# Kernel optimization log

Measured on AMD Instinct MI355X. Metric: run time of the kernel, lower is better.

Reference implementation:

```python
import jax, jax.numpy as jnp
import numpy as np

C = 64  # channels fixed by module

def conv1x1(x, W, b):
    # x: [B,C,H,W], W: [C_out,C_in], b: [C_out]
    return jnp.einsum('bchw,oc->bohw', x, W) + b[None, :, None, None]

def setup_inputs() -> dict:
    key = jax.random.key(0)
    ks = jax.random.split(key, 16)
    B, H, W = 4, 64, 64
    inp = {
        'x_latter': jax.random.normal(ks[0], (B, C, H, W), jnp.float32),
        'x': jax.random.normal(ks[1], (B, C, H, W), jnp.float32),
    }
    scale = 1.0 / np.sqrt(C)
    names = ['high', 'low', 'value', 'e_conv', 'mid', 'latter']
    for i, n in enumerate(names):
        inp[f'W_{n}'] = jax.random.normal(ks[2 + 2 * i], (C, C), jnp.float32) * scale
        inp[f'b_{n}'] = jax.random.normal(ks[3 + 2 * i], (C,), jnp.float32) * 0.01
    return inp

def reference(x_latter, x, W_high, b_high, W_low, b_low, W_value, b_value,
              W_e_conv, b_e_conv, W_mid, b_mid, W_latter, b_latter):
    b, c, h, w = x_latter.shape
    hw = h * w
    # stage 1: channel-normalized spatial attention
    xl_hi = conv1x1(x_latter, W_high, b_high).reshape(b, c, hw)          # [b,c,hw]
    x_low = conv1x1(x, W_low, b_low).reshape(b, c, hw).transpose(0, 2, 1)  # [b,hw,c]
    p = jnp.einsum('bnc,bcm->bnm', x_low, xl_hi)                          # [b,hw,hw]
    p = jax.nn.softmax(p, axis=1)  # torch Softmax(dim=1) over first hw axis
    v = conv1x1(x, W_value, b_value).reshape(b, c, hw).transpose(0, 2, 1)  # [b,hw,c]
    e = jnp.einsum('bnm,bmc->bnc', p, v) + x_low                          # [b,hw,c]
    e = e.transpose(0, 2, 1).reshape(b, c, h, w)                          # [b,c,h,w]
    e = conv1x1(e, W_e_conv, b_e_conv).reshape(b, c, hw)                  # [b,c,hw]
    # stage 2: channel-channel attention
    xl2 = conv1x1(x_latter, W_latter, b_latter).reshape(b, c, hw).transpose(0, 2, 1)  # [b,hw,c]
    t = jnp.einsum('bcn,bnd->bcd', e, xl2)                                # [b,c,c]
    t = jax.nn.softmax(t, axis=1)
    x_mid = conv1x1(x, W_mid, b_mid).reshape(b, c, hw).transpose(0, 2, 1)  # [b,hw,c]
    out = jnp.einsum('bnc,bcd->bnd', x_mid, t)                            # [b,hw,c]
    return out.transpose(0, 2, 1).reshape(b, c, h, w)
```

## Files before the change

### kernel.cpp

```cpp
#include <hip/hip_runtime.h>
#include <math.h>

#define BATCH 4
#define CH 64
#define HW 4096

typedef __attribute__((ext_vector_type(8))) short short8;
typedef __attribute__((ext_vector_type(4))) float f32x4;
typedef __attribute__((ext_vector_type(4))) float float4v;

#define MFMA(a, b, c) __builtin_amdgcn_mfma_f32_16x16x32_bf16(a, b, c, 0, 0, 0)

__device__ __forceinline__ short f2bf(float f) {
    unsigned u = __builtin_bit_cast(unsigned, f);
    u += 0x7fffu + ((u >> 16) & 1u);
    return (short)(u >> 16);
}
__device__ __forceinline__ float bf2f(short s) {
    unsigned u = ((unsigned)(unsigned short)s) << 16;
    return __builtin_bit_cast(float, u);
}
__device__ __forceinline__ void gld16(const short* g, short* l) {
    __builtin_amdgcn_global_load_lds(
        (const __attribute__((address_space(1))) unsigned int*)g,
        (__attribute__((address_space(3))) unsigned int*)l, 16, 0, 0);
}

__global__ __launch_bounds__(256) void splitX(
    const float* __restrict__ x, const float* __restrict__ xl,
    short* __restrict__ XFh, short* __restrict__ XFl)
{
    int src = blockIdx.z, b = blockIdx.y, bx = blockIdx.x;
    const float* X = src ? xl : x;
    int t = threadIdx.x, wv = t >> 6, ln = t & 63;
    int nt = bx * 4 + wv;
    int n = (nt << 4) + (ln & 15);
    int g = ln >> 4;
    size_t sb = ((size_t)(src * BATCH + b) * 256 + nt) * 2;
    #pragma unroll
    for (int kt = 0; kt < 2; kt++) {
        short8 h, l;
        #pragma unroll
        for (int j = 0; j < 8; j++) {
            float v = X[(size_t)(b * 64 + kt * 32 + g * 8 + j) * HW + n];
            short hh = f2bf(v);
            h[j] = hh;
            l[j] = f2bf(v - bf2f(hh));
        }
        *(short8*)(XFh + (sb + kt) * 512 + (size_t)ln * 8) = h;
        *(short8*)(XFl + (sb + kt) * 512 + (size_t)ln * 8) = l;
    }
}

__global__ __launch_bounds__(256) void convm(
    const short* __restrict__ XFh, const short* __restrict__ XFl,
    const float* __restrict__ Wlow, const float* __restrict__ blow,
    const float* __restrict__ Wval, const float* __restrict__ bval,
    const float* __restrict__ Wmid, const float* __restrict__ bmid,
    const float* __restrict__ Wlat, const float* __restrict__ blat,
    const float* __restrict__ Whigh, const float* __restrict__ bhigh,
    float* __restrict__ XLOW, float* __restrict__ XMID, float* __restrict__ XL2,
    short* __restrict__ PAh, short* __restrict__ PAl,
    short* __restrict__ PBh, short* __restrict__ PBl,
    short* __restrict__ PVh, short* __restrict__ PVl)
{
    int mode = blockIdx.z, b = blockIdx.y, bx = blockIdx.x;
    const float* W; const float* bias; int src;
    switch (mode) {
        case 0:  W = Wlow;  bias = blow;  src = 0; break;
        case 1:  W = Wval;  bias = bval;  src = 0; break;
        case 2:  W = Wmid;  bias = bmid;  src = 0; break;
        case 3:  W = Wlat;  bias = blat;  src = 1; break;
        default: W = Whigh; bias = bhigh; src = 1; break;
    }
    int t = threadIdx.x, wv = t >> 6, ln = t & 63;
    int row = ln & 15, g = ln >> 4;

    short8 Wh[4][2], Wlo[4][2];
    #pragma unroll
    for (int ot = 0; ot < 4; ot++)
        #pragma unroll
        for (int kt = 0; kt < 2; kt++) {
            const float* wp = W + (ot * 16 + row) * 64 + kt * 32 + g * 8;
            short8 h, l;
            #pragma unroll
            for (int j = 0; j < 8; j++) {
                float v = wp[j];
                short hh = f2bf(v);
                h[j] = hh;
                l[j] = f2bf(v - bf2f(hh));
            }
            Wh[ot][kt] = h; Wlo[ot][kt] = l;
        }

    int nt = bx * 4 + wv;
    size_t xb = ((size_t)(src * BATCH + b) * 256 + nt) * 2;
    short8 Bh[2], Bl[2];
    #pragma unroll
    for (int kt = 0; kt < 2; kt++) {
        Bh[kt] = *(const short8*)(XFh + (xb + kt) * 512 + (size_t)ln * 8);
        Bl[kt] = *(const short8*)(XFl + (xb + kt) * 512 + (size_t)ln * 8);
    }

    f32x4 acc[4];
    #pragma unroll
    for (int ot = 0; ot < 4; ot++) {
        #pragma unroll
        for (int r = 0; r < 4; r++) acc[ot][r] = bias[ot * 16 + g * 4 + r];
    }
    #pragma unroll
    for (int ot = 0; ot < 4; ot++)
        #pragma unroll
        for (int kt = 0; kt < 2; kt++) {
            acc[ot] = MFMA(Wh[ot][kt], Bh[kt], acc[ot]);
            acc[ot] = MFMA(Wh[ot][kt], Bl[kt], acc[ot]);
            acc[ot] = MFMA(Wlo[ot][kt], Bh[kt], acc[ot]);
        }

    __shared__ float Ld[64][65];
    #pragma unroll
    for (int ot = 0; ot < 4; ot++)
        #pragma unroll
        for (int r = 0; r < 4; r++)
            Ld[wv * 16 + (ln & 15)][ot * 16 + g * 4 + r] = acc[ot][r];
    __syncthreads();

    int n0 = bx * 64;
    if (mode == 0 || mode == 2 || mode == 3) {
        float* outp = (mode == 0) ? XLOW : (mode == 2) ? XMID : XL2;
        int n = t >> 2, o0 = (t & 3) * 16;
        float vout[16];
        #pragma unroll
        for (int k = 0; k < 16; k++) vout[k] = Ld[n][o0 + k];
        float* gp = outp + ((size_t)b * HW + n0 + n) * 64 + o0;
        #pragma unroll
        for (int k = 0; k < 4; k++)
            *(float4v*)(gp + k * 4) = *(float4v*)(vout + k * 4);
    }
    if (mode == 0 || mode == 4) {
        short* Ph = (mode == 0) ? PAh : PBh;
        short* Pl = (mode == 0) ? PAl : PBl;
        #pragma unroll
        for (int kt = 0; kt < 2; kt++) {
            short8 h, l;
            #pragma unroll
            for (int j = 0; j < 8; j++) {
                float v = Ld[wv * 16 + (ln & 15)][kt * 32 + g * 8 + j];
                short hh = f2bf(v);
                h[j] = hh;
                l[j] = f2bf(v - bf2f(hh));
            }
            size_t blob = (((size_t)b * 256 + bx * 4 + wv) * 2 + kt) * 512 + (size_t)ln * 8;
            *(short8*)(Ph + blob) = h;
            *(short8*)(Pl + blob) = l;
        }
    }
    if (mode == 1) {
        int ktm_l = wv >> 1;
        int ct0 = (wv & 1) * 2;
        #pragma unroll
        for (int cc = 0; cc < 2; cc++) {
            int ct = ct0 + cc;
            int c = ct * 16 + (ln & 15);
            short8 h, l;
            #pragma unroll
            for (int j = 0; j < 8; j++) {
                float v = Ld[(ktm_l * 2 + (j >> 2)) * 16 + g * 4 + (j & 3)][c];
                short hh = f2bf(v);
                h[j] = hh;
                l[j] = f2bf(v - bf2f(hh));
            }
            size_t blob = (((size_t)b * 128 + bx * 2 + ktm_l) * 4 + ct) * 512 + (size_t)ln * 8;
            *(short8*)(PVh + blob) = h;
            *(short8*)(PVl + blob) = l;
        }
    }
}

__global__ __launch_bounds__(256) void zpass2(
    const short* __restrict__ PAh, const short* __restrict__ PAl,
    const short* __restrict__ PBh, const short* __restrict__ PBl,
    float* __restrict__ Zp)
{
    int bid = blockIdx.x;
    int sw = (bid & 7) * 128 + (bid >> 3);
    int mchunk = sw & 63, nc = (sw >> 6) & 3, b = sw >> 8;
    int t = threadIdx.x, wv = t >> 6, ln = t & 63;
    short8 bh[4][2], bl[4][2];
    #pragma unroll
    for (int msub = 0; msub < 4; msub++)
        #pragma unroll
        for (int kt = 0; kt < 2; kt++) {
            size_t o = ((size_t)(b * 256 + mchunk * 4 + msub) * 2 + kt) * 512 + ln * 8;
            bh[msub][kt] = *(const short8*)(PBh + o);
            bl[msub][kt] = *(const short8*)(PBl + o);
        }
    float zacc[4] = {0.f, 0.f, 0.f, 0.f};
    for (int s = 0; s < 16; s++) {
        int nt = nc * 64 + s * 4 + wv;
        size_t ab = ((size_t)(b * 256 + nt) * 2) * 512 + ln * 8;
        short8 ah0 = *(const short8*)(PAh + ab);
        short8 ah1 = *(const short8*)(PAh + ab + 512);
        short8 al0 = *(const short8*)(PAl + ab);
        short8 al1 = *(const short8*)(PAl + ab + 512);
        #pragma unroll
        for (int msub = 0; msub < 4; msub++) {
            f32x4 acc = {0.f, 0.f, 0.f, 0.f};
            acc = MFMA(ah0, bh[msub][0], acc);
            acc = MFMA(ah1, bh[msub][1], acc);
            acc = MFMA(ah0, bl[msub][0], acc);
            acc = MFMA(ah1, bl[msub][1], acc);
            acc = MFMA(al0, bh[msub][0], acc);
            acc = MFMA(al1, bh[msub][1], acc);
            zacc[msub] += __expf(acc[0]) + __expf(acc[1]) + __expf(acc[2]) + __expf(acc[3]);
        }
    }
    #pragma unroll
    for (int msub = 0; msub < 4; msub++) {
        zacc[msub] += __shfl_xor(zacc[msub], 16, 64);
        zacc[msub] += __shfl_xor(zacc[msub], 32, 64);
    }
    __shared__ float sZ[4][64];
    if (ln < 16) {
        #pragma unroll
        for (int msub = 0; msub < 4; msub++) sZ[wv][msub * 16 + ln] = zacc[msub];
    }
    __syncthreads();
    if (t < 64) {
        float z = sZ[0][t] + sZ[1][t] + sZ[2][t] + sZ[3][t];
        Zp[((size_t)(b * 4 + nc)) * 4096 + mchunk * 64 + t] = z;
    }
}

__global__ __launch_bounds__(256) void zmerge(
    const float* __restrict__ Zp, float* __restrict__ Zi)
{
    int gi = blockIdx.x * 256 + threadIdx.x;
    int b = gi >> 12, m = gi & 4095;
    float z = 0.f;
    #pragma unroll
    for (int nc2 = 0; nc2 < 4; nc2++) z += Zp[((size_t)(b * 4 + nc2)) * 4096 + m];
    Zi[gi] = 1.f / z;
}

__global__ __launch_bounds__(256) void epass5(
    const short* __restrict__ PAh, const short* __restrict__ PAl,
    const short* __restrict__ PBh, const short* __restrict__ PBl,
    const short* __restrict__ PVh, const short* __restrict__ PVl,
    const float* __restrict__ Zi, float* __restrict__ Ep)
{
    int bid = blockIdx.x;
    int sw = (bid & 7) * 64 + (bid >> 3);
    int b = sw >> 7, mseg = (sw >> 5) & 3, nb = sw & 31;
    int t = threadIdx.x, wv = t >> 6, ln = t & 63;
    int lnm = ln & 15, lnr = ln >> 4;

    __shared__ __align__(16) short sB[2][2][4096];
    __shared__ __align__(16) short sV[2][2][4096];
    __shared__ float sZi[1024];

    for (int k = t; k < 1024; k += 256) sZi[k] = Zi[b * 4096 + mseg * 1024 + k];
    __syncthreads();

    short8 Lh[2][2], Ll[2][2];
    #pragma unroll
    for (int rt = 0; rt < 2; rt++)
        #pragma unroll
        for (int kt = 0; kt < 2; kt++) {
            int nt = nb * 8 + wv * 2 + rt;
            size_t base = ((size_t)(b * 256 + nt) * 2 + kt) * 512 + ln * 8;
            Lh[rt][kt] = *(const short8*)(PAh + base);
            Ll[rt][kt] = *(const short8*)(PAl + base);
        }

    f32x4 acc_e[2][4];
    #pragma unroll
    for (int rt = 0; rt < 2; rt++)
        #pragma unroll
        for (int ct = 0; ct < 4; ct++) acc_e[rt][ct] = (f32x4){0.f, 0.f, 0.f, 0.f};

    const int mc0 = mseg * 16;
    #define STAGE(bufi, ii) { \
        size_t bb = (size_t)b * 262144 + (size_t)(mc0 + (ii)) * 4096; \
        gld16(PBh + bb + t * 8,        &sB[bufi][0][wv * 512]); \
        gld16(PBh + bb + 2048 + t * 8, &sB[bufi][0][2048 + wv * 512]); \
        gld16(PBl + bb + t * 8,        &sB[bufi][1][wv * 512]); \
        gld16(PBl + bb + 2048 + t * 8, &sB[bufi][1][2048 + wv * 512]); \
        gld16(PVh + bb + t * 8,        &sV[bufi][0][wv * 512]); \
        gld16(PVh + bb + 2048 + t * 8, &sV[bufi][0][2048 + wv * 512]); \
        gld16(PVl + bb + t * 8,        &sV[bufi][1][wv * 512]); \
        gld16(PVl + bb + 2048 + t * 8, &sV[bufi][1][2048 + wv * 512]); }

    STAGE(0, 0);
    for (int i = 0; i < 16; i++) {
        int cur = i & 1;
        __builtin_amdgcn_s_barrier();
        if (i < 15) {
            STAGE(cur ^ 1, i + 1);
            asm volatile("s_waitcnt vmcnt(8)" ::: "memory");
        } else {
            asm volatile("s_waitcnt vmcnt(0)" ::: "memory");
        }
        __builtin_amdgcn_sched_barrier(0);

        f32x4 wf[2][4];
        #pragma unroll
        for (int msub = 0; msub < 4; msub++) {
            const short8 bh0 = *(const short8*)&sB[cur][0][(msub * 2 + 0) * 512 + ln * 8];
            const short8 bh1 = *(const short8*)&sB[cur][0][(msub * 2 + 1) * 512 + ln * 8];
            const short8 bl0 = *(const short8*)&sB[cur][1][(msub * 2 + 0) * 512 + ln * 8];
            const short8 bl1 = *(const short8*)&sB[cur][1][(msub * 2 + 1) * 512 + ln * 8];
            const f32x4 vz = *(const f32x4*)&sZi[i * 64 + msub * 16 + lnr * 4];
            #pragma unroll
            for (int rt = 0; rt < 2; rt++) {
                f32x4 acc = {0.f, 0.f, 0.f, 0.f};
                acc = MFMA(bh0, Lh[rt][0], acc);
                acc = MFMA(bh1, Lh[rt][1], acc);
                acc = MFMA(bh0, Ll[rt][0], acc);
                acc = MFMA(bh1, Ll[rt][1], acc);
                acc = MFMA(bl0, Lh[rt][0], acc);
                acc = MFMA(bl1, Lh[rt][1], acc);
                #pragma unroll
                for (int r = 0; r < 4; r++)
                    wf[rt][msub][r] = __expf(acc[r]) * vz[r];
            }
        }
        short8 pah[2][2], pal[2][2];
        #pragma unroll
        for (int rt = 0; rt < 2; rt++)
            #pragma unroll
            for (int kt = 0; kt < 2; kt++) {
                short8 h, l;
                #pragma unroll
                for (int j = 0; j < 8; j++) {
                    float w = wf[rt][kt * 2 + (j >> 2)][j & 3];
                    short hh = f2bf(w);
                    h[j] = hh;
                    l[j] = f2bf(w - bf2f(hh));
                }
                pah[rt][kt] = h; pal[rt][kt] = l;
            }
        #pragma unroll
        for (int kt = 0; kt < 2; kt++) {
            #pragma unroll
            for (int ct = 0; ct < 4; ct++) {
                const short8 vh = *(const short8*)&sV[cur][0][(kt * 4 + ct) * 512 + ln * 8];
                const short8 vl = *(const short8*)&sV[cur][1][(kt * 4 + ct) * 512 + ln * 8];
                acc_e[0][ct] = MFMA(pah[0][kt], vh, acc_e[0][ct]);
                acc_e[0][ct] = MFMA(pah[0][kt], vl, acc_e[0][ct]);
                acc_e[0][ct] = MFMA(pal[0][kt], vh, acc_e[0][ct]);
                acc_e[1][ct] = MFMA(pah[1][kt], vh, acc_e[1][ct]);
                acc_e[1][ct] = MFMA(pah[1][kt], vl, acc_e[1][ct]);
                acc_e[1][ct] = MFMA(pal[1][kt], vh, acc_e[1][ct]);
            }
        }
    }
    #undef STAGE

    float* ep = Ep + ((size_t)mseg * BATCH + b) * HW * 64;
    #pragma unroll
    for (int rt = 0; rt < 2; rt++) {
        int n0 = (nb * 8 + wv * 2 + rt) * 16 + lnr * 4;
        #pragma unroll
        for (int ct = 0; ct < 4; ct++) {
            #pragma unroll
            for (int r = 0; r < 4; r++)
                ep[(size_t)(n0 + r) * 64 + ct * 16 + lnm] = acc_e[rt][ct][r];
        }
    }
}

__global__ __launch_bounds__(256) void econv5(
    const float* __restrict__ Ep, const float* __restrict__ XLOW,
    const float* __restrict__ W, const float* __restrict__ bias,
    float* __restrict__ E2)
{
    const size_t SEG = (size_t)BATCH * HW * 64;
    int b = blockIdx.y, n0 = blockIdx.x * 64, t = threadIdx.x;
    __shared__ float Wl[64][64];
    __shared__ float El[64][65];
    for (int i = t; i < 4096; i += 256) Wl[i >> 6][i & 63] = W[i];
    for (int i = t; i < 4096; i += 256) {
        int nl = i >> 6, c = i & 63;
        size_t idx = ((size_t)b * HW + n0 + nl) * 64 + c;
        El[nl][c] = XLOW[idx] + Ep[idx] + Ep[SEG + idx] + Ep[2 * SEG + idx] + Ep[3 * SEG + idx];
    }
    __syncthreads();
    int nl = t & 63, og = t >> 6;
    for (int k = 0; k < 16; k++) {
        int o = og * 16 + k;
        float a0 = bias[o], a1 = 0.f, a2 = 0.f, a3 = 0.f;
        #pragma unroll
        for (int c = 0; c < 64; c += 4) {
            a0 += Wl[o][c]     * El[nl][c];
            a1 += Wl[o][c + 1] * El[nl][c + 1];
            a2 += Wl[o][c + 2] * El[nl][c + 2];
            a3 += Wl[o][c + 3] * El[nl][c + 3];
        }
        E2[((size_t)b * 64 + o) * HW + n0 + nl] = (a0 + a1) + (a2 + a3);
    }
}

__global__ __launch_bounds__(1024) void tmat(
    const float* __restrict__ E2, const float* __restrict__ XL2, float* __restrict__ T)
{
    int b = blockIdx.y, c = blockIdx.x, t = threadIdx.x;
    int d = t & 63, nl = t >> 6;
    const float* e = E2 + ((size_t)b * 64 + c) * HW;
    const float* x2 = XL2 + (size_t)b * HW * 64;
    float a0 = 0.f, a1 = 0.f;
    #pragma unroll 4
    for (int k = 0; k < 256; k += 2) {
        int na = k * 16 + nl, nb2 = na + 16;
        a0 += e[na] * x2[(size_t)na * 64 + d];
        a1 += e[nb2] * x2[(size_t)nb2 * 64 + d];
    }
    __shared__ float red[16][64];
    red[nl][d] = a0 + a1;
    __syncthreads();
    if (t < 64) {
        float s = 0.f;
        #pragma unroll
        for (int j = 0; j < 16; j++) s += red[j][t];
        T[((size_t)b * 64 + c) * 64 + t] = s;
    }
}

__global__ __launch_bounds__(64) void softT(
    const float* __restrict__ T, float* __restrict__ Ts)
{
    int d = blockIdx.x, b = blockIdx.y, c = threadIdx.x;
    float v = T[((size_t)b * 64 + c) * 64 + d];
    float M = v;
    #pragma unroll
    for (int o = 32; o > 0; o >>= 1) M = fmaxf(M, __shfl_xor(M, o, 64));
    float ez = __expf(v - M);
    float Z = ez;
    #pragma unroll
    for (int o = 32; o > 0; o >>= 1) Z += __shfl_xor(Z, o, 64);
    Ts[((size_t)b * 64 + c) * 64 + d] = ez / Z;
}

__global__ __launch_bounds__(256) void outk(
    const float* __restrict__ XMID, const float* __restrict__ Ts, float* __restrict__ out)
{
    int b = blockIdx.y, n0 = blockIdx.x * 64, t = threadIdx.x;
    __shared__ float Xm[64][65];
    __shared__ float Tl[64][64];
    for (int i = t; i < 4096; i += 256) {
        int nl = i >> 6, c = i & 63;
        Xm[nl][c] = XMID[((size_t)b * HW + n0 + nl) * 64 + c];
    }
    for (int i = t; i < 4096; i += 256) Tl[i >> 6][i & 63] = Ts[(size_t)b * 4096 + i];
    __syncthreads();
    int nl = t & 63, dg = t >> 6;
    float accs[16];
    #pragma unroll
    for (int k = 0; k < 16; k++) accs[k] = 0.f;
    for (int c = 0; c < 64; c++) {
        float xv = Xm[nl][c];
        #pragma unroll
        for (int k = 0; k < 16; k++) accs[k] += xv * Tl[c][dg * 16 + k];
    }
    #pragma unroll
    for (int k = 0; k < 16; k++) {
        int d = dg * 16 + k;
        out[((size_t)b * 64 + d) * HW + n0 + nl] = accs[k];
    }
}

extern "C" void kernel_launch(void* const* d_in, const int* in_sizes, int n_in,
                              void* d_out, int out_size, void* d_ws, size_t ws_size,
                              hipStream_t stream)
{
    const float* x_latter = (const float*)d_in[0];
    const float* x        = (const float*)d_in[1];
    const float* W_high = (const float*)d_in[2];  const float* b_high = (const float*)d_in[3];
    const float* W_low  = (const float*)d_in[4];  const float* b_low  = (const float*)d_in[5];
    const float* W_val  = (const float*)d_in[6];  const float* b_val  = (const float*)d_in[7];
    const float* W_ec   = (const float*)d_in[8];  const float* b_ec   = (const float*)d_in[9];
    const float* W_mid  = (const float*)d_in[10]; const float* b_mid  = (const float*)d_in[11];
    const float* W_lat  = (const float*)d_in[12]; const float* b_lat  = (const float*)d_in[13];
    float* outp = (float*)d_out;

    const size_t MAT = (size_t)BATCH * CH * HW;
    float* ws = (float*)d_ws;
    size_t off = 0;
    float* XLOW = ws + off; off += MAT;
    float* XMID = ws + off; off += MAT;
    float* XL2  = ws + off; off += MAT;
    float* Ep   = ws + off; off += 4 * MAT;
    float* Zp   = ws + off; off += (size_t)BATCH * 4 * HW;
    float* Zic  = ws + off; off += (size_t)BATCH * HW;
    float* T    = ws + off; off += (size_t)BATCH * 64 * 64;
    float* Ts   = ws + off; off += (size_t)BATCH * 64 * 64;
    short* sp = (short*)(ws + off);
    short* PAh = sp; sp += MAT;
    short* PAl = sp; sp += MAT;
    short* PBh = sp; sp += MAT;
    short* PBl = sp; sp += MAT;
    short* PVh = sp; sp += MAT;
    short* PVl = sp; sp += MAT;
    float* E2  = (float*)PAh;
    short* XFh = (short*)Ep;
    short* XFl = XFh + 2 * BATCH * 262144;

    splitX<<<dim3(64, BATCH, 2), 256, 0, stream>>>(x, x_latter, XFh, XFl);
    convm<<<dim3(64, BATCH, 5), 256, 0, stream>>>(
        XFh, XFl, W_low, b_low, W_val, b_val, W_mid, b_mid, W_lat, b_lat,
        W_high, b_high, XLOW, XMID, XL2, PAh, PAl, PBh, PBl, PVh, PVl);
    zpass2<<<dim3(1024), 256, 0, stream>>>(PAh, PAl, PBh, PBl, Zp);
    zmerge<<<dim3(64), 256, 0, stream>>>(Zp, Zic);
    epass5<<<dim3(512), 256, 0, stream>>>(PAh, PAl, PBh, PBl, PVh, PVl, Zic, Ep);
    econv5<<<dim3(64, BATCH), 256, 0, stream>>>(Ep, XLOW, W_ec, b_ec, E2);
    tmat<<<dim3(64, BATCH), 1024, 0, stream>>>(E2, XL2, T);
    softT<<<dim3(64, BATCH), 64, 0, stream>>>(T, Ts);
    outk<<<dim3(64, BATCH), 256, 0, stream>>>(XMID, Ts, outp);
}
```

Before: 153.1 us.

## Double per-wave row tiles in attention pass and fold Z merge into it

```diff
diff --git a/kernel.cpp b/kernel.cpp
--- a/kernel.cpp
+++ b/kernel.cpp
@@ -232,26 +232,15 @@
     }
 }
 
-__global__ __launch_bounds__(256) void zmerge(
-    const float* __restrict__ Zp, float* __restrict__ Zi)
-{
-    int gi = blockIdx.x * 256 + threadIdx.x;
-    int b = gi >> 12, m = gi & 4095;
-    float z = 0.f;
-    #pragma unroll
-    for (int nc2 = 0; nc2 < 4; nc2++) z += Zp[((size_t)(b * 4 + nc2)) * 4096 + m];
-    Zi[gi] = 1.f / z;
-}
-
-__global__ __launch_bounds__(256) void epass5(
+__global__ __launch_bounds__(256, 1) void epass6(
     const short* __restrict__ PAh, const short* __restrict__ PAl,
     const short* __restrict__ PBh, const short* __restrict__ PBl,
     const short* __restrict__ PVh, const short* __restrict__ PVl,
-    const float* __restrict__ Zi, float* __restrict__ Ep)
+    const float* __restrict__ Zp, float* __restrict__ Ep)
 {
     int bid = blockIdx.x;
-    int sw = (bid & 7) * 64 + (bid >> 3);
-    int b = sw >> 7, mseg = (sw >> 5) & 3, nb = sw & 31;
+    int sw = (bid & 7) * 32 + (bid >> 3);
+    int b = sw >> 6, mseg = (sw >> 4) & 3, nb = sw & 15;
     int t = threadIdx.x, wv = t >> 6, ln = t & 63;
     int lnm = ln & 15, lnr = ln >> 4;
 
@@ -259,23 +248,29 @@
     __shared__ __align__(16) short sV[2][2][4096];
     __shared__ float sZi[1024];
 
-    for (int k = t; k < 1024; k += 256) sZi[k] = Zi[b * 4096 + mseg * 1024 + k];
-    __syncthreads();
-
-    short8 Lh[2][2], Ll[2][2];
-    #pragma unroll
-    for (int rt = 0; rt < 2; rt++)
+    for (int k = t; k < 1024; k += 256) {
+        int m = mseg * 1024 + k;
+        float z = Zp[((size_t)(b * 4 + 0)) * 4096 + m]
+                + Zp[((size_t)(b * 4 + 1)) * 4096 + m]
+                + Zp[((size_t)(b * 4 + 2)) * 4096 + m]
+                + Zp[((size_t)(b * 4 + 3)) * 4096 + m];
+        sZi[k] = 1.f / z;
+    }
+
+    short8 Lh[4][2], Ll[4][2];
+    #pragma unroll
+    for (int rt = 0; rt < 4; rt++)
         #pragma unroll
         for (int kt = 0; kt < 2; kt++) {
-            int nt = nb * 8 + wv * 2 + rt;
+            int nt = nb * 16 + wv * 4 + rt;
             size_t base = ((size_t)(b * 256 + nt) * 2 + kt) * 512 + ln * 8;
             Lh[rt][kt] = *(const short8*)(PAh + base);
             Ll[rt][kt] = *(const short8*)(PAl + base);
         }
 
-    f32x4 acc_e[2][4];
-    #pragma unroll
-    for (int rt = 0; rt < 2; rt++)
+    f32x4 acc_e[4][4];
+    #pragma unroll
+    for (int rt = 0; rt < 4; rt++)
         #pragma unroll
         for (int ct = 0; ct < 4; ct++) acc_e[rt][ct] = (f32x4){0.f, 0.f, 0.f, 0.f};
 
@@ -292,6 +287,7 @@
         gld16(PVl + bb + 2048 + t * 8, &sV[bufi][1][2048 + wv * 512]); }
 
     STAGE(0, 0);
+    __syncthreads();
     for (int i = 0; i < 16; i++) {
         int cur = i & 1;
         __builtin_amdgcn_s_barrier();
@@ -303,55 +299,54 @@
         }
         __builtin_amdgcn_sched_barrier(0);
 
-        f32x4 wf[2][4];
-        #pragma unroll
-        for (int msub = 0; msub < 4; msub++) {
-            const short8 bh0 = *(const short8*)&sB[cur][0][(msub * 2 + 0) * 512 + ln * 8];
-            const short8 bh1 = *(const short8*)&sB[cur][0][(msub * 2 + 1) * 512 + ln * 8];
-            const short8 bl0 = *(const short8*)&sB[cur][1][(msub * 2 + 0) * 512 + ln * 8];
-            const short8 bl1 = *(const short8*)&sB[cur][1][(msub * 2 + 1) * 512 + ln * 8];
-            const f32x4 vz = *(const f32x4*)&sZi[i * 64 + msub * 16 + lnr * 4];
-            #pragma unroll
-            for (int rt = 0; rt < 2; rt++) {
-                f32x4 acc = {0.f, 0.f, 0.f, 0.f};
-                acc = MFMA(bh0, Lh[rt][0], acc);
-                acc = MFMA(bh1, Lh[rt][1], acc);
-                acc = MFMA(bh0, Ll[rt][0], acc);
-                acc = MFMA(bh1, Ll[rt][1], acc);
-                acc = MFMA(bl0, Lh[rt][0], acc);
-                acc = MFMA(bl1, Lh[rt][1], acc);
+        #pragma unroll
+        for (int ktm = 0; ktm < 2; ktm++) {
+            f32x4 wf[4][2];
+            #pragma unroll
+            for (int ms = 0; ms < 2; ms++) {
+                int msub = ktm * 2 + ms;
+                const short8 bh0 = *(const short8*)&sB[cur][0][(msub * 2 + 0) * 512 + ln * 8];
+                const short8 bh1 = *(const short8*)&sB[cur][0][(msub * 2 + 1) * 512 + ln * 8];
+                const short8 bl0 = *(const short8*)&sB[cur][1][(msub * 2 + 0) * 512 + ln * 8];
+                const short8 bl1 = *(const short8*)&sB[cur][1][(msub * 2 + 1) * 512 + ln * 8];
+                const f32x4 vz = *(const f32x4*)&sZi[i * 64 + msub * 16 + lnr * 4];
                 #pragma unroll
-                for (int r = 0; r < 4; r++)
-                    wf[rt][msub][r] = __expf(acc[r]) * vz[r];
+                for (int rt = 0; rt < 4; rt++) {
+                    f32x4 acc = {0.f, 0.f, 0.f, 0.f};
+                    acc = MFMA(bh0, Lh[rt][0], acc);
+                    acc = MFMA(bh1, Lh[rt][1], acc);
+                    acc = MFMA(bh0, Ll[rt][0], acc);
+                    acc = MFMA(bh1, Ll[rt][1], acc);
+                    acc = MFMA(bl0, Lh[rt][0], acc);
+                    acc = MFMA(bl1, Lh[rt][1], acc);
+                    #pragma unroll
+                    for (int r = 0; r < 4; r++)
+                        wf[rt][ms][r] = __expf(acc[r]) * vz[r];
+                }
             }
-        }
-        short8 pah[2][2], pal[2][2];
-        #pragma unroll
-        for (int rt = 0; rt < 2; rt++)
-            #pragma unroll
-            for (int kt = 0; kt < 2; kt++) {
+            short8 pah[4], pal[4];
+            #pragma unroll
+            for (int rt = 0; rt < 4; rt++) {
                 short8 h, l;
                 #pragma unroll
                 for (int j = 0; j < 8; j++) {
-                    float w = wf[rt][kt * 2 + (j >> 2)][j & 3];
+                    float w = wf[rt][j >> 2][j & 3];
                     short hh = f2bf(w);
                     h[j] = hh;
                     l[j] = f2bf(w - bf2f(hh));
                 }
-                pah[rt][kt] = h; pal[rt][kt] = l;
+                pah[rt] = h; pal[rt] = l;
             }
-        #pragma unroll
-        for (int kt = 0; kt < 2; kt++) {
             #pragma unroll
             for (int ct = 0; ct < 4; ct++) {
-                const short8 vh = *(const short8*)&sV[cur][0][(kt * 4 + ct) * 512 + ln * 8];
-                const short8 vl = *(const short8*)&sV[cur][1][(kt * 4 + ct) * 512 + ln * 8];
-                acc_e[0][ct] = MFMA(pah[0][kt], vh, acc_e[0][ct]);
-                acc_e[0][ct] = MFMA(pah[0][kt], vl, acc_e[0][ct]);
-                acc_e[0][ct] = MFMA(pal[0][kt], vh, acc_e[0][ct]);
-                acc_e[1][ct] = MFMA(pah[1][kt], vh, acc_e[1][ct]);
-                acc_e[1][ct] = MFMA(pah[1][kt], vl, acc_e[1][ct]);
-                acc_e[1][ct] = MFMA(pal[1][kt], vh, acc_e[1][ct]);
+                const short8 vh = *(const short8*)&sV[cur][0][(ktm * 4 + ct) * 512 + ln * 8];
+                const short8 vl = *(const short8*)&sV[cur][1][(ktm * 4 + ct) * 512 + ln * 8];
+                #pragma unroll
+                for (int rt = 0; rt < 4; rt++) {
+                    acc_e[rt][ct] = MFMA(pah[rt], vh, acc_e[rt][ct]);
+                    acc_e[rt][ct] = MFMA(pah[rt], vl, acc_e[rt][ct]);
+                    acc_e[rt][ct] = MFMA(pal[rt], vh, acc_e[rt][ct]);
+                }
             }
         }
     }
@@ -359,8 +354,8 @@
 
     float* ep = Ep + ((size_t)mseg * BATCH + b) * HW * 64;
     #pragma unroll
-    for (int rt = 0; rt < 2; rt++) {
-        int n0 = (nb * 8 + wv * 2 + rt) * 16 + lnr * 4;
+    for (int rt = 0; rt < 4; rt++) {
+        int n0 = (nb * 16 + wv * 4 + rt) * 16 + lnr * 4;
         #pragma unroll
         for (int ct = 0; ct < 4; ct++) {
             #pragma unroll
@@ -491,7 +486,6 @@
     float* XL2  = ws + off; off += MAT;
     float* Ep   = ws + off; off += 4 * MAT;
     float* Zp   = ws + off; off += (size_t)BATCH * 4 * HW;
-    float* Zic  = ws + off; off += (size_t)BATCH * HW;
     float* T    = ws + off; off += (size_t)BATCH * 64 * 64;
     float* Ts   = ws + off; off += (size_t)BATCH * 64 * 64;
     short* sp = (short*)(ws + off);
@@ -510,8 +504,7 @@
         XFh, XFl, W_low, b_low, W_val, b_val, W_mid, b_mid, W_lat, b_lat,
         W_high, b_high, XLOW, XMID, XL2, PAh, PAl, PBh, PBl, PVh, PVl);
     zpass2<<<dim3(1024), 256, 0, stream>>>(PAh, PAl, PBh, PBl, Zp);
-    zmerge<<<dim3(64), 256, 0, stream>>>(Zp, Zic);
-    epass5<<<dim3(512), 256, 0, stream>>>(PAh, PAl, PBh, PBl, PVh, PVl, Zic, Ep);
+    epass6<<<dim3(256), 256, 0, stream>>>(PAh, PAl, PBh, PBl, PVh, PVl, Zp, Ep);
     econv5<<<dim3(64, BATCH), 256, 0, stream>>>(Ep, XLOW, W_ec, b_ec, E2);
     tmat<<<dim3(64, BATCH), 1024, 0, stream>>>(E2, XL2, T);
     softT<<<dim3(64, BATCH), 64, 0, stream>>>(T, Ts);
```

Result: slower. 156.4 us (+2.2%).
